# Optimization experiments

Hardware: AMD Instinct MI355X
Metric: run time of the kernel (lower is better)

The kernel has to match this reference:

```python
import jax, jax.numpy as jnp
import numpy as np

N = 50000          # nodes
E = 1600000        # edges (avg degree 32)
DIMS = [128, 128, 128, 64]  # in_features + hidden_dims


def setup_inputs() -> dict:
    key = jax.random.key(0)
    ks = jax.random.split(key, 10)
    x = jax.random.normal(ks[0], (N, DIMS[0]), dtype=jnp.float32)
    edge_index = jax.random.randint(ks[1], (2, E), 0, N, dtype=jnp.int64)
    edge_weight = jax.random.uniform(ks[2], (E,), dtype=jnp.float32)
    params = {}
    for i in range(3):
        fan_in, fan_out = DIMS[i], DIMS[i + 1]
        scale = jnp.sqrt(6.0 / (fan_in + fan_out))  # glorot as in PyG GCNConv lin
        params[f"W{i+1}"] = jax.random.uniform(ks[3 + i], (fan_in, fan_out), jnp.float32, -scale, scale)
        params[f"b{i+1}"] = jnp.zeros((fan_out,), jnp.float32)
    return dict(x=x, edge_index=edge_index, edge_weight=edge_weight, **params)


def gcn_norm(edge_index, edge_weight, n):
    # PyG gcn_norm: add self-loops (weight 1), symmetric deg^-1/2 normalization
    src, dst = edge_index[0], edge_index[1]
    loop = jnp.arange(n, dtype=src.dtype)
    src = jnp.concatenate([src, loop])
    dst = jnp.concatenate([dst, loop])
    ew = jnp.concatenate([edge_weight, jnp.ones((n,), edge_weight.dtype)])
    deg = jax.ops.segment_sum(ew, dst, num_segments=n)  # degree at target
    dinv = jnp.where(deg > 0, jax.lax.rsqrt(jnp.maximum(deg, 1e-30)), 0.0)
    return src, dst, dinv[src] * ew * dinv[dst]


def gcn_conv(x, W, b, src, dst, norm, n):
    h = x @ W                                   # [N, out]
    msg = h[src] * norm[:, None]                # gather + edge scale
    agg = jax.ops.segment_sum(msg, dst, num_segments=n)  # scatter-add to targets
    return agg + b


def reference(x, edge_index, edge_weight, W1, b1, W2, b2, W3, b3):
    n = x.shape[0]
    src, dst, norm = gcn_norm(edge_index, edge_weight, n)
    x = jax.nn.relu(gcn_conv(x, W1, b1, src, dst, norm, n))
    x = jax.nn.relu(gcn_conv(x, W2, b2, src, dst, norm, n))
    return gcn_conv(x, W3, b3, src, dst, norm, n)
```

## Files before the change

kernel.cpp:

```cpp
#include <hip/hip_runtime.h>
#include <hip/hip_bf16.h>
#include <hip/hip_fp16.h>


#define K_IN 128
#define FIX_SCALE 8388608.0f
#define CE 4096

typedef _Float16 f16x8 __attribute__((ext_vector_type(8)));
typedef float f32x4 __attribute__((ext_vector_type(4)));

__global__ __launch_bounds__(1024) void part_count_wt(
    const int* __restrict__ dst, int* __restrict__ counts,
    unsigned short* __restrict__ lrank, int nb, int nblk, int e,
    const float* __restrict__ W1, const float* __restrict__ W2,
    const float* __restrict__ W3, _Float16* __restrict__ Wt1,
    _Float16* __restrict__ Wt2, _Float16* __restrict__ Wt3) {
    int blk = blockIdx.x;
    if (blk >= nblk) {
        int i = (blk - nblk) * 1024 + threadIdx.x;
        if (i < 128 * 128) {
            int k = i >> 7, nn = i & 127;
            Wt1[(size_t)nn * 128 + k] = (_Float16)W1[i];
        } else if (i < 2 * 128 * 128) {
            int j = i - 128 * 128, k = j >> 7, nn = j & 127;
            Wt2[(size_t)nn * 128 + k] = (_Float16)W2[j];
        } else if (i < 2 * 128 * 128 + 64 * 128) {
            int l = i - 2 * 128 * 128, k = l >> 6, nn = l & 63;
            Wt3[(size_t)nn * 128 + k] = (_Float16)W3[l];
        }
        return;
    }
    __shared__ int c[256];
    int t = threadIdx.x;
    for (int i = t; i < nb; i += 1024) c[i] = 0;
    __syncthreads();
    int b0 = blk * CE;
#pragma unroll
    for (int j = 0; j < 4; j++) {
        int i = b0 + j * 1024 + t;
        if (i < e) {
            int b = dst[i] >> 8;
            int r = atomicAdd(&c[b], 1);
            lrank[i] = (unsigned short)r;
        }
    }
    __syncthreads();
    for (int i = t; i < nb; i += 1024) counts[(size_t)i * nblk + blk] = c[i];
}

__global__ __launch_bounds__(256) void reduce_kernel(const int* __restrict__ v,
                                                     int* __restrict__ bs, int m) {
    __shared__ int s[256];
    int t = threadIdx.x, i = blockIdx.x * 256 + t;
    s[t] = (i < m) ? v[i] : 0;
    __syncthreads();
    for (int off = 128; off > 0; off >>= 1) {
        if (t < off) s[t] += s[t + off];
        __syncthreads();
    }
    if (t == 0) bs[blockIdx.x] = s[0];
}

__global__ __launch_bounds__(1024) void scanb1024(const int* __restrict__ bs,
                                                  int* __restrict__ bo, int nbb) {
    __shared__ int s[1024];
    int t = threadIdx.x;
    s[t] = (t < nbb) ? bs[t] : 0;
    __syncthreads();
    for (int off = 1; off < 1024; off <<= 1) {
        int cur = s[t];
        int add = (t >= off) ? s[t - off] : 0;
        __syncthreads();
        s[t] = cur + add;
        __syncthreads();
    }
    if (t < nbb) bo[t] = (t == 0) ? 0 : s[t - 1];
}

__global__ __launch_bounds__(256) void scanw_kernel(const int* __restrict__ v,
                                                    const int* __restrict__ bo,
                                                    int* __restrict__ outp, int m) {
    __shared__ int s[256];
    int t = threadIdx.x, i = blockIdx.x * 256 + t;
    int c = (i < m) ? v[i] : 0;
    s[t] = c;
    __syncthreads();
    for (int off = 1; off < 256; off <<= 1) {
        int cur = s[t];
        int add = (t >= off) ? s[t - off] : 0;
        __syncthreads();
        s[t] = cur + add;
        __syncthreads();
    }
    if (i < m) outp[i] = bo[blockIdx.x] + (s[t] - c);
}

__global__ __launch_bounds__(1024) void part_scatter(const int* __restrict__ src,
                                                     const int* __restrict__ dst,
                                                     const float* __restrict__ ew,
                                                     const int* __restrict__ base,
                                                     const unsigned short* __restrict__ lrank,
                                                     int2* __restrict__ arr1,
                                                     int nblk, int e) {
    int t = threadIdx.x, blk = blockIdx.x;
    int b0 = blk * CE;
#pragma unroll
    for (int j = 0; j < 4; j++) {
        int i = b0 + j * 1024 + t;
        if (i < e) {
            int d = dst[i];
            int b = d >> 8;
            int pos = base[(size_t)b * nblk + blk] + lrank[i];
            arr1[pos] = make_int2((src[i] << 8) | (d & 255), __float_as_int(ew[i]));
        }
    }
}

__global__ __launch_bounds__(1024) void bucket_csr(const int2* __restrict__ arr1,
                                                   const int* __restrict__ base,
                                                   unsigned short* __restrict__ rank2,
                                                   float* __restrict__ dinv,
                                                   int* __restrict__ row_ptr,
                                                   int2* __restrict__ ep,
                                                   int nb, int nblk, int n, int e) {
    __shared__ unsigned long long pk[256];
    __shared__ int nbase[256];
    __shared__ float ldsdinv[256];
    __shared__ int ss[256];
    int t = threadIdx.x, b = blockIdx.x;
    int beg = base[(size_t)b * nblk];
    int end = (b + 1 < nb) ? base[(size_t)(b + 1) * nblk] : e;
    if (t < 256) pk[t] = 0ULL;
    __syncthreads();
    for (int i = beg + t; i < end; i += 1024) {
        int2 a = arr1[i];
        int ld = a.x & 255;
        float w = __int_as_float(a.y);
        unsigned long long fx = (unsigned long long)(unsigned int)(w * FIX_SCALE + 0.5f);
        unsigned long long old = atomicAdd(&pk[ld], (fx << 32) | 1ULL);
        rank2[i] = (unsigned short)(old & 0xffffffffULL);
    }
    __syncthreads();
    int cnt = (t < 256) ? (int)(pk[t] & 0xffffffffULL) : 0;
    if (t < 256) ss[t] = cnt;
    __syncthreads();
    for (int off = 1; off < 256; off <<= 1) {
        int cur = 0, add = 0;
        if (t < 256) { cur = ss[t]; add = (t >= off) ? ss[t - off] : 0; }
        __syncthreads();
        if (t < 256) ss[t] = cur + add;
        __syncthreads();
    }
    if (t < 256) {
        nbase[t] = ss[t] - cnt;
        int d = b * 256 + t;
        if (d < n) {
            float dv = rsqrtf(1.0f + (float)(unsigned int)(pk[t] >> 32) * (1.0f / FIX_SCALE));
            dinv[d] = dv;
            ldsdinv[t] = dv;
            row_ptr[d] = beg + nbase[t];
        }
    }
    __syncthreads();
    for (int i = beg + t; i < end; i += 1024) {
        int2 a = arr1[i];
        int ld = a.x & 255;
        int pos = beg + nbase[ld] + rank2[i];
        float w = __int_as_float(a.y) * ldsdinv[ld];
        ep[pos] = make_int2(a.x >> 8, __float_as_int(w));
    }
}

template <int NOUT, bool XF16, bool FUSEVAL>
__global__ __launch_bounds__(256) void mfma_gemm(const void* __restrict__ Xv,
                                                 const _Float16* __restrict__ Wt,
                                                 _Float16* __restrict__ H, int n,
                                                 int gGemm, int vblk,
                                                 int2* __restrict__ ep,
                                                 const float* __restrict__ dinv,
                                                 int* __restrict__ row_ptr, int e) {
    constexpr int CTW = NOUT / 64;
    __shared__ _Float16 Xs[64][136];
    __shared__ _Float16 Ws[NOUT][136];
    int t = threadIdx.x;
    if (FUSEVAL && (int)blockIdx.x >= gGemm) {
        int vb = blockIdx.x - gGemm;
        if (vb == 0 && t == 0) row_ptr[n] = e;
        for (int i = vb * 256 + t; i < e; i += vblk * 256) {
            int2 a = ep[i];
            float w = __int_as_float(a.y) * dinv[a.x];
            ep[i] = make_int2(a.x << 8, __float_as_int(w));
        }
        return;
    }
    int row0 = blockIdx.x * 64;

    for (int i = t * 8; i < NOUT * K_IN; i += 2048) {
        int nn = i >> 7, k = i & 127;
        *(uint4*)&Ws[nn][k] = *(const uint4*)&Wt[i];
    }
    if (XF16) {
        const _Float16* X = (const _Float16*)Xv;
        for (int i = t * 8; i < 64 * K_IN; i += 2048) {
            int r = i >> 7, k = i & 127;
            int row = row0 + r;
            uint4 v = make_uint4(0u, 0u, 0u, 0u);
            if (row < n) v = *(const uint4*)(X + (size_t)row * K_IN + k);
            *(uint4*)&Xs[r][k] = v;
        }
    } else {
        const float* X = (const float*)Xv;
        for (int i = t * 4; i < 64 * K_IN; i += 1024) {
            int r = i >> 7, k = i & 127;
            int row = row0 + r;
            float4 x4 = make_float4(0.f, 0.f, 0.f, 0.f);
            if (row < n) x4 = *(const float4*)(X + (size_t)row * K_IN + k);
            union { _Float16 h[4]; uint2 u; } uu;
            uu.h[0] = (_Float16)x4.x; uu.h[1] = (_Float16)x4.y;
            uu.h[2] = (_Float16)x4.z; uu.h[3] = (_Float16)x4.w;
            *(uint2*)&Xs[r][k] = uu.u;
        }
    }
    __syncthreads();

    int lane = t & 63, w = t >> 6;
    int m = lane & 15, g = lane >> 4;
    f32x4 acc[4][CTW];
#pragma unroll
    for (int mt = 0; mt < 4; mt++)
#pragma unroll
        for (int ct = 0; ct < CTW; ct++) acc[mt][ct] = (f32x4){0.f, 0.f, 0.f, 0.f};

#pragma unroll
    for (int kt = 0; kt < 4; kt++) {
        int kb = kt * 32 + g * 8;
        f16x8 a[4];
#pragma unroll
        for (int mt = 0; mt < 4; mt++) a[mt] = *(const f16x8*)&Xs[mt * 16 + m][kb];
#pragma unroll
        for (int ct = 0; ct < CTW; ct++) {
            int nn = w * (16 * CTW) + ct * 16 + m;
            f16x8 b = *(const f16x8*)&Ws[nn][kb];
#pragma unroll
            for (int mt = 0; mt < 4; mt++)
                acc[mt][ct] = __builtin_amdgcn_mfma_f32_16x16x32_f16(a[mt], b, acc[mt][ct], 0, 0, 0);
        }
    }

#pragma unroll
    for (int mt = 0; mt < 4; mt++) {
#pragma unroll
        for (int r = 0; r < 4; r++) {
            int row = row0 + mt * 16 + g * 4 + r;
            if (row < n) {
#pragma unroll
                for (int ct = 0; ct < CTW; ct++)
                    H[(size_t)row * NOUT + w * (16 * CTW) + ct * 16 + m] =
                        (_Float16)acc[mt][ct][r];
            }
        }
    }
}

template <int F, bool RELU, bool OF16>
__global__ __launch_bounds__(256) void agg_kernel(const __half* __restrict__ H,
                                                  const int* __restrict__ row_ptr,
                                                  const int2* __restrict__ ep,
                                                  const float* __restrict__ dinv,
                                                  const float* __restrict__ bias,
                                                  void* __restrict__ outv, int n) {
    constexpr int UN = 24;
    int wid = threadIdx.x >> 6;
    int lane = threadIdx.x & 63;
    int node = blockIdx.x * 4 + wid;
    if (node >= n) return;

    int start = __builtin_amdgcn_readfirstlane(row_ptr[node]);
    int end   = __builtin_amdgcn_readfirstlane(row_ptr[node + 1]);
    float di = dinv[node];
    float sw = di * di;

    const unsigned lb = (unsigned)lane * (F == 128 ? 4u : 2u);

    float a0, a1;
    if (F == 128) {
        float2 s2 = __half22float2(((const __half2*)(H + (size_t)node * 128))[lane]);
        a0 = s2.x * sw; a1 = s2.y * sw;
    } else {
        a0 = __half2float(H[(size_t)node * 64 + lane]) * sw; a1 = 0.f;
    }

    int len = end - start;
    int nf = len / UN;
    for (int b = 0; b < nf; b++) {
        int p0 = start + b * UN;
        int2 e[UN];
#pragma unroll
        for (int u = 0; u < UN; u++) e[u] = ep[p0 + u];
        __half2 v2[UN];
        __half v1[UN];
#pragma unroll
        for (int u = 0; u < UN; u++) {
            unsigned off = (unsigned)e[u].x;
            if (F == 64) off >>= 1;
            if (F == 128) v2[u] = *(const __half2*)((const char*)H + (off + lb));
            else          v1[u] = *(const __half*)((const char*)H + (off + lb));
        }
#pragma unroll
        for (int u = 0; u < UN; u++) {
            float w = __int_as_float(e[u].y);
            if (F == 128) {
                float2 f = __half22float2(v2[u]);
                a0 += w * f.x; a1 += w * f.y;
            } else {
                a0 += w * __half2float(v1[u]);
            }
        }
    }
    int base = start + nf * UN;
    if (base < end) {
        int2 e[UN];
#pragma unroll
        for (int u = 0; u < UN; u++) {
            int p = base + u;
            int q = (p < end) ? p : end - 1;
            int2 t2 = ep[q];
            if (p >= end) t2.y = 0;
            e[u] = t2;
        }
        __half2 v2[UN];
        __half v1[UN];
#pragma unroll
        for (int u = 0; u < UN; u++) {
            unsigned off = (unsigned)e[u].x;
            if (F == 64) off >>= 1;
            if (F == 128) v2[u] = *(const __half2*)((const char*)H + (off + lb));
            else          v1[u] = *(const __half*)((const char*)H + (off + lb));
        }
#pragma unroll
        for (int u = 0; u < UN; u++) {
            float w = __int_as_float(e[u].y);
            if (F == 128) {
                float2 f = __half22float2(v2[u]);
                a0 += w * f.x; a1 += w * f.y;
            } else {
                a0 += w * __half2float(v1[u]);
            }
        }
    }

    if (F == 128) {
        float o0 = a0 + bias[lane * 2];
        float o1 = a1 + bias[lane * 2 + 1];
        if (RELU) { o0 = fmaxf(o0, 0.f); o1 = fmaxf(o1, 0.f); }
        if (OF16) {
            ((__half2*)outv)[(size_t)node * 64 + lane] = __floats2half2_rn(o0, o1);
        } else {
            *(float2*)((float*)outv + (size_t)node * 128 + lane * 2) = make_float2(o0, o1);
        }
    } else {
        float o = a0 + bias[lane];
        if (RELU) o = fmaxf(o, 0.f);
        if (OF16) ((__half*)outv)[(size_t)node * 64 + lane] = __float2half(o);
        else      ((float*)outv)[(size_t)node * 64 + lane] = o;
    }
}


extern "C" void kernel_launch(void* const* d_in, const int* in_sizes, int n_in,
                              void* d_out, int out_size, void* d_ws, size_t ws_size,
                              hipStream_t stream) {
    const float* x   = (const float*)d_in[0];
    const int*   ei  = (const int*)d_in[1];
    const float* ew  = (const float*)d_in[2];
    const float* W1  = (const float*)d_in[3];
    const float* b1  = (const float*)d_in[4];
    const float* W2  = (const float*)d_in[5];
    const float* b2  = (const float*)d_in[6];
    const float* W3  = (const float*)d_in[7];
    const float* b3  = (const float*)d_in[8];
    float* out = (float*)d_out;

    const int N = in_sizes[0] / K_IN;
    const int E = in_sizes[2];
    const int* src = ei;
    const int* dst = ei + E;

    const int NB   = (N + 255) >> 8;
    const int NBLK = (E + CE - 1) / CE;
    const int M    = NB * NBLK;
    const int NBB  = (M + 255) / 256;
    const int NWT  = (2 * 128 * 128 + 64 * 128 + 1023) / 1024;
    const int VBLK = 1024;

    char* w = (char*)d_ws;
    auto alloc = [&](size_t bytes) {
        void* p = (void*)w;
        w += (bytes + 255) & ~(size_t)255;
        return p;
    };
    int*            counts = (int*)alloc((size_t)M * 4);
    int*            base   = (int*)alloc((size_t)M * 4);
    int*            bsM    = (int*)alloc((size_t)NBB * 4);
    int*            boM    = (int*)alloc((size_t)NBB * 4);
    unsigned short* lrank  = (unsigned short*)alloc((size_t)E * 2);
    int2*           arr1   = (int2*)alloc((size_t)E * 8);
    float*          dinv   = (float*)alloc((size_t)N * 4);
    int*            row_ptr= (int*)alloc((size_t)(N + 1) * 4);
    int2*           ep     = (int2*)alloc((size_t)E * 8);
    _Float16*       Wt1    = (_Float16*)alloc(128 * 128 * 2);
    _Float16*       Wt2    = (_Float16*)alloc(128 * 128 * 2);
    _Float16*       Wt3    = (_Float16*)alloc(64 * 128 * 2);
    _Float16*       bufH   = (_Float16*)alloc((size_t)N * 128 * 2);
    _Float16*       bufX   = (_Float16*)alloc((size_t)N * 128 * 2);

    int gGemm = (N + 63) / 64;
    int gAgg  = (N + 3) / 4;

    part_count_wt<<<NBLK + NWT, 1024, 0, stream>>>(dst, counts, lrank, NB, NBLK, E,
                                                   W1, W2, W3, Wt1, Wt2, Wt3);
    reduce_kernel<<<NBB, 256, 0, stream>>>(counts, bsM, M);
    scanb1024<<<1, 1024, 0, stream>>>(bsM, boM, NBB);
    scanw_kernel<<<NBB, 256, 0, stream>>>(counts, boM, base, M);
    part_scatter<<<NBLK, 1024, 0, stream>>>(src, dst, ew, base, lrank, arr1, NBLK, E);
    bucket_csr<<<NB, 1024, 0, stream>>>(arr1, base, lrank, dinv, row_ptr, ep,
                                        NB, NBLK, N, E);

    mfma_gemm<128, false, true><<<gGemm + VBLK, 256, 0, stream>>>(
        x, Wt1, bufH, N, gGemm, VBLK, ep, dinv, row_ptr, E);
    agg_kernel<128, true, true><<<gAgg, 256, 0, stream>>>((const __half*)bufH, row_ptr, ep,
                                                          dinv, b1, bufX, N);
    mfma_gemm<128, true, false><<<gGemm, 256, 0, stream>>>(
        bufX, Wt2, bufH, N, gGemm, 0, nullptr, nullptr, nullptr, 0);
    agg_kernel<128, true, true><<<gAgg, 256, 0, stream>>>((const __half*)bufH, row_ptr, ep,
                                                          dinv, b2, bufX, N);
    mfma_gemm<64, true, false><<<gGemm, 256, 0, stream>>>(
        bufX, Wt3, bufH, N, gGemm, 0, nullptr, nullptr, nullptr, 0);
    agg_kernel<64, false, false><<<gAgg, 256, 0, stream>>>((const __half*)bufH, row_ptr, ep,
                                                           dinv, b3, out, N);
}
```

Baseline: 321.6 us.

## Split wavefront into edge groups with 16-byte feature gathers and shuffle reduction

```diff
diff --git a/kernel.cpp b/kernel.cpp
--- a/kernel.cpp
+++ b/kernel.cpp
@@ -270,7 +270,9 @@
                                                   const float* __restrict__ dinv,
                                                   const float* __restrict__ bias,
                                                   void* __restrict__ outv, int n) {
-    constexpr int UN = 24;
+    constexpr int LPE = (F == 128) ? 16 : 8;
+    constexpr int EPW = 64 / LPE;
+    constexpr int UNC = (F == 128) ? 4 : 2;
     int wid = threadIdx.x >> 6;
     int lane = threadIdx.x & 63;
     int node = blockIdx.x * 4 + wid;
@@ -281,89 +283,92 @@
     float di = dinv[node];
     float sw = di * di;
 
-    const unsigned lb = (unsigned)lane * (F == 128 ? 4u : 2u);
-
-    float a0, a1;
-    if (F == 128) {
-        float2 s2 = __half22float2(((const __half2*)(H + (size_t)node * 128))[lane]);
-        a0 = s2.x * sw; a1 = s2.y * sw;
-    } else {
-        a0 = __half2float(H[(size_t)node * 64 + lane]) * sw; a1 = 0.f;
+    int g  = lane / LPE;
+    int fl = lane & (LPE - 1);
+    const unsigned flb = (unsigned)fl * 16u;
+    const char* Hb = (const char*)H;
+
+    float acc[8];
+    {
+        uint4 sv = *(const uint4*)(Hb + (size_t)node * (F * 2) + flb);
+        const __half2* sh = (const __half2*)&sv;
+        float gm = (g == 0) ? sw : 0.0f;
+#pragma unroll
+        for (int j = 0; j < 4; j++) {
+            float2 f = __half22float2(sh[j]);
+            acc[2 * j]     = gm * f.x;
+            acc[2 * j + 1] = gm * f.y;
+        }
     }
 
     int len = end - start;
-    int nf = len / UN;
-    for (int b = 0; b < nf; b++) {
-        int p0 = start + b * UN;
-        int2 e[UN];
-#pragma unroll
-        for (int u = 0; u < UN; u++) e[u] = ep[p0 + u];
-        __half2 v2[UN];
-        __half v1[UN];
-#pragma unroll
-        for (int u = 0; u < UN; u++) {
-            unsigned off = (unsigned)e[u].x;
-            if (F == 64) off >>= 1;
-            if (F == 128) v2[u] = *(const __half2*)((const char*)H + (off + lb));
-            else          v1[u] = *(const __half*)((const char*)H + (off + lb));
-        }
-#pragma unroll
-        for (int u = 0; u < UN; u++) {
-            float w = __int_as_float(e[u].y);
-            if (F == 128) {
-                float2 f = __half22float2(v2[u]);
-                a0 += w * f.x; a1 += w * f.y;
-            } else {
-                a0 += w * __half2float(v1[u]);
+    int nch = (len + EPW - 1) / EPW;
+    int pg  = start + g;
+
+    auto ldep = [&](int c) -> int2 {
+        int p = pg + c * EPW;
+        int q = (p < end) ? p : (end - 1);
+        int2 t = ep[q];
+        if (p >= end) t.y = 0;
+        return t;
+    };
+
+    if (nch > 0) {
+        int2 e[UNC];
+#pragma unroll
+        for (int u = 0; u < UNC; u++) e[u] = ldep(u);
+        for (int c0 = 0; c0 < nch; c0 += UNC) {
+            uint4 v[UNC];
+#pragma unroll
+            for (int u = 0; u < UNC; u++) {
+                unsigned off = (unsigned)e[u].x;
+                if (F == 64) off >>= 1;
+                v[u] = *(const uint4*)(Hb + (off + flb));
             }
-        }
-    }
-    int base = start + nf * UN;
-    if (base < end) {
-        int2 e[UN];
-#pragma unroll
-        for (int u = 0; u < UN; u++) {
-            int p = base + u;
-            int q = (p < end) ? p : end - 1;
-            int2 t2 = ep[q];
-            if (p >= end) t2.y = 0;
-            e[u] = t2;
-        }
-        __half2 v2[UN];
-        __half v1[UN];
-#pragma unroll
-        for (int u = 0; u < UN; u++) {
-            unsigned off = (unsigned)e[u].x;
-            if (F == 64) off >>= 1;
-            if (F == 128) v2[u] = *(const __half2*)((const char*)H + (off + lb));
-            else          v1[u] = *(const __half*)((const char*)H + (off + lb));
-        }
-#pragma unroll
-        for (int u = 0; u < UN; u++) {
-            float w = __int_as_float(e[u].y);
-            if (F == 128) {
-                float2 f = __half22float2(v2[u]);
-                a0 += w * f.x; a1 += w * f.y;
-            } else {
-                a0 += w * __half2float(v1[u]);
+            int2 e2[UNC];
+#pragma unroll
+            for (int u = 0; u < UNC; u++) e2[u] = ldep(c0 + UNC + u);
+#pragma unroll
+            for (int u = 0; u < UNC; u++) {
+                float w = __int_as_float(e[u].y);
+                const __half2* h2 = (const __half2*)&v[u];
+#pragma unroll
+                for (int j = 0; j < 4; j++) {
+                    float2 f = __half22float2(h2[j]);
+                    acc[2 * j]     = fmaf(w, f.x, acc[2 * j]);
+                    acc[2 * j + 1] = fmaf(w, f.y, acc[2 * j + 1]);
+                }
             }
-        }
-    }
-
-    if (F == 128) {
-        float o0 = a0 + bias[lane * 2];
-        float o1 = a1 + bias[lane * 2 + 1];
-        if (RELU) { o0 = fmaxf(o0, 0.f); o1 = fmaxf(o1, 0.f); }
+#pragma unroll
+            for (int u = 0; u < UNC; u++) e[u] = e2[u];
+        }
+    }
+
+#pragma unroll
+    for (int mask = LPE; mask < 64; mask <<= 1) {
+#pragma unroll
+        for (int j = 0; j < 8; j++) acc[j] += __shfl_xor(acc[j], mask, 64);
+    }
+
+    if (g == 0) {
+        float4 b0 = *(const float4*)(bias + fl * 8);
+        float4 b1 = *(const float4*)(bias + fl * 8 + 4);
+        float o[8] = {acc[0] + b0.x, acc[1] + b0.y, acc[2] + b0.z, acc[3] + b0.w,
+                      acc[4] + b1.x, acc[5] + b1.y, acc[6] + b1.z, acc[7] + b1.w};
+        if (RELU) {
+#pragma unroll
+            for (int j = 0; j < 8; j++) o[j] = fmaxf(o[j], 0.0f);
+        }
         if (OF16) {
-            ((__half2*)outv)[(size_t)node * 64 + lane] = __floats2half2_rn(o0, o1);
+            union { __half2 h[4]; uint4 u; } r;
+#pragma unroll
+            for (int j = 0; j < 4; j++) r.h[j] = __floats2half2_rn(o[2 * j], o[2 * j + 1]);
+            *(uint4*)((char*)outv + (size_t)node * (F * 2) + flb) = r.u;
         } else {
-            *(float2*)((float*)outv + (size_t)node * 128 + lane * 2) = make_float2(o0, o1);
-        }
-    } else {
-        float o = a0 + bias[lane];
-        if (RELU) o = fmaxf(o, 0.f);
-        if (OF16) ((__half*)outv)[(size_t)node * 64 + lane] = __float2half(o);
-        else      ((float*)outv)[(size_t)node * 64 + lane] = o;
+            float* op = (float*)outv + (size_t)node * F + fl * 8;
+            *(float4*)op       = make_float4(o[0], o[1], o[2], o[3]);
+            *(float4*)(op + 4) = make_float4(o[4], o[5], o[6], o[7]);
+        }
     }
 }
 
```

Result: faster. 311.6 us (-3.1%).

## Stage partition scatter and CSR edge writes through shared memory for coalescing

Applied to the files above, without the earlier changes.

```diff
diff --git a/kernel.cpp b/kernel.cpp
--- a/kernel.cpp
+++ b/kernel.cpp
@@ -100,23 +100,56 @@
                                                      const int* __restrict__ dst,
                                                      const float* __restrict__ ew,
                                                      const int* __restrict__ base,
+                                                     const int* __restrict__ counts,
                                                      const unsigned short* __restrict__ lrank,
                                                      int2* __restrict__ arr1,
-                                                     int nblk, int e) {
+                                                     int nb, int nblk, int e) {
+    __shared__ int hs[256];
+    __shared__ int lbase[256];
+    __shared__ int gb[256];
+    __shared__ unsigned char bb[CE];
+    __shared__ int2 buf[CE];
     int t = threadIdx.x, blk = blockIdx.x;
+
+    if (t < 256) hs[t] = (t < nb) ? counts[(size_t)t * nblk + blk] : 0;
+    __syncthreads();
+    for (int off = 1; off < 256; off <<= 1) {
+        int cur = 0, add = 0;
+        if (t < 256) { cur = hs[t]; add = (t >= off) ? hs[t - off] : 0; }
+        __syncthreads();
+        if (t < 256) hs[t] = cur + add;
+        __syncthreads();
+    }
+    if (t < 256) {
+        int cnt = (t < nb) ? counts[(size_t)t * nblk + blk] : 0;
+        int lb = hs[t] - cnt;
+        lbase[t] = lb;
+        gb[t] = ((t < nb) ? base[(size_t)t * nblk + blk] : 0) - lb;
+    }
+    __syncthreads();
+
     int b0 = blk * CE;
+    int nloc = e - b0; if (nloc > CE) nloc = CE;
 #pragma unroll
     for (int j = 0; j < 4; j++) {
         int i = b0 + j * 1024 + t;
         if (i < e) {
             int d = dst[i];
             int b = d >> 8;
-            int pos = base[(size_t)b * nblk + blk] + lrank[i];
-            arr1[pos] = make_int2((src[i] << 8) | (d & 255), __float_as_int(ew[i]));
-        }
-    }
-}
-
+            int slot = lbase[b] + lrank[i];
+            buf[slot] = make_int2((src[i] << 8) | (d & 255), __float_as_int(ew[i]));
+            bb[slot] = (unsigned char)b;
+        }
+    }
+    __syncthreads();
+#pragma unroll
+    for (int j = 0; j < 4; j++) {
+        int s = j * 1024 + t;
+        if (s < nloc) arr1[gb[bb[s]] + s] = buf[s];
+    }
+}
+
+#define EPCAP 10240
 __global__ __launch_bounds__(1024) void bucket_csr(const int2* __restrict__ arr1,
                                                    const int* __restrict__ base,
                                                    unsigned short* __restrict__ rank2,
@@ -128,6 +161,7 @@
     __shared__ int nbase[256];
     __shared__ float ldsdinv[256];
     __shared__ int ss[256];
+    __shared__ int2 eps[EPCAP];
     int t = threadIdx.x, b = blockIdx.x;
     int beg = base[(size_t)b * nblk];
     int end = (b + 1 < nb) ? base[(size_t)(b + 1) * nblk] : e;
@@ -163,12 +197,24 @@
         }
     }
     __syncthreads();
-    for (int i = beg + t; i < end; i += 1024) {
-        int2 a = arr1[i];
-        int ld = a.x & 255;
-        int pos = beg + nbase[ld] + rank2[i];
-        float w = __int_as_float(a.y) * ldsdinv[ld];
-        ep[pos] = make_int2(a.x >> 8, __float_as_int(w));
+    int tot = end - beg;
+    if (tot <= EPCAP) {
+        for (int i = beg + t; i < end; i += 1024) {
+            int2 a = arr1[i];
+            int ld = a.x & 255;
+            float w = __int_as_float(a.y) * ldsdinv[ld];
+            eps[nbase[ld] + rank2[i]] = make_int2(a.x >> 8, __float_as_int(w));
+        }
+        __syncthreads();
+        for (int j = t; j < tot; j += 1024) ep[beg + j] = eps[j];
+    } else {
+        for (int i = beg + t; i < end; i += 1024) {
+            int2 a = arr1[i];
+            int ld = a.x & 255;
+            int pos = beg + nbase[ld] + rank2[i];
+            float w = __int_as_float(a.y) * ldsdinv[ld];
+            ep[pos] = make_int2(a.x >> 8, __float_as_int(w));
+        }
     }
 }
 
@@ -423,7 +469,8 @@
     reduce_kernel<<<NBB, 256, 0, stream>>>(counts, bsM, M);
     scanb1024<<<1, 1024, 0, stream>>>(bsM, boM, NBB);
     scanw_kernel<<<NBB, 256, 0, stream>>>(counts, boM, base, M);
-    part_scatter<<<NBLK, 1024, 0, stream>>>(src, dst, ew, base, lrank, arr1, NBLK, E);
+    part_scatter<<<NBLK, 1024, 0, stream>>>(src, dst, ew, base, counts, lrank,
+                                            arr1, NB, NBLK, E);
     bucket_csr<<<NB, 1024, 0, stream>>>(arr1, base, lrank, dinv, row_ptr, ep,
                                         NB, NBLK, N, E);
 
```

Result: faster. 294.0 us (-8.6%).
